# Kernel optimization log

Measured on AMD Instinct MI355X. Metric: run time of the kernel, lower is better.

The kernel has to match this reference:

```python
import jax, jax.numpy as jnp
import numpy as np
import math

NUM_CLASSES = 80
ANCHORS = [(12.0, 16.0), (19.0, 36.0), (40.0, 28.0)]
ANGLES = [-np.pi/3, -np.pi/6, 0.0, np.pi/6, np.pi/3, np.pi/2]
STRIDE = 8.0
SCALE_XY = 1.05
IGNORE_THRESH = 0.5
MASKED_ANCHORS = np.array([[w/STRIDE, h/STRIDE, a] for (w, h) in ANCHORS for a in ANGLES], dtype=np.float32)  # [18,3]
NA = MASKED_ANCHORS.shape[0]
LAMBDA_COORD, LAMBDA_CONF, LAMBDA_CLS = 1.0, 10.0, 1.0
FOCAL_ALPHA, FOCAL_GAMMA = 0.25, 2.0


def setup_inputs() -> dict:
    key = jax.random.key(0)
    B, G, nT = 8, 76, 240
    k1, k2, k3, k4, k5, k6 = jax.random.split(key, 6)
    output = jax.random.normal(k1, (B, NA * (NUM_CLASSES + 6), G, G), jnp.float32) * 0.1
    tb = jax.random.randint(k2, (nT,), 0, B).astype(jnp.float32)
    tl = jax.random.randint(k3, (nT,), 0, NUM_CLASSES).astype(jnp.float32)
    txy = jax.random.uniform(k4, (nT, 2), minval=0.02, maxval=0.98)
    twh = jax.random.uniform(k5, (nT, 2), minval=0.05, maxval=0.4)
    tang = jax.random.uniform(k6, (nT, 1), minval=-np.pi/2, maxval=np.pi/2)
    target = jnp.concatenate([tb[:, None], tl[:, None], txy, twh, tang], axis=-1)  # [nT,7]
    return {"output": output, "target": target}


def _smooth_l1(x, y):
    d = jnp.abs(x - y)
    return jnp.where(d < 1.0, 0.5 * d * d, d - 0.5)


def _bce(p, t):
    eps = 1e-7
    p = jnp.clip(p, eps, 1.0 - eps)
    return -(t * jnp.log(p) + (1.0 - t) * jnp.log(1.0 - p))


def _focal(p, t):
    loss = _bce(p, t)
    p_t = t * p + (1.0 - t) * (1.0 - p)
    alpha_f = t * FOCAL_ALPHA + (1.0 - t) * (1.0 - FOCAL_ALPHA)
    return loss * alpha_f * (1.0 - p_t) ** FOCAL_GAMMA


def _ciou(pb, tb):
    # pb, tb: [N,5] (cx, cy, w, h, angle) in grid units
    p1, p2 = pb[:, :2] - pb[:, 2:4] / 2, pb[:, :2] + pb[:, 2:4] / 2
    t1, t2 = tb[:, :2] - tb[:, 2:4] / 2, tb[:, :2] + tb[:, 2:4] / 2
    w1, h1 = p2[:, 0] - p1[:, 0], p2[:, 1] - p1[:, 1]
    w2, h2 = t2[:, 0] - t1[:, 0], t2[:, 1] - t1[:, 1]
    area1, area2 = w1 * h1, w2 * h2
    c1, c2 = (p1 + p2) / 2, (t1 + t2) / 2
    inter = jnp.clip(jnp.minimum(p2, t2) - jnp.maximum(p1, t1), 0.0)
    inter_area = inter[:, 0] * inter[:, 1]
    inter_diag = jnp.sum((c2 - c1) ** 2, axis=-1)
    outer = jnp.clip(jnp.maximum(p2, t2) - jnp.minimum(p1, t1), 0.0)
    outer_diag = outer[:, 0] ** 2 + outer[:, 1] ** 2
    union = area1 + area2 - inter_area
    u = inter_diag / outer_diag
    iou = inter_area / union
    v = (4.0 / math.pi ** 2) * (jnp.arctan(w2 / h2) - jnp.arctan(w1 / h1)) ** 2
    alpha = jax.lax.stop_gradient(v / ((1.0 - iou) + v))
    ciou = jnp.clip(iou - (u + alpha * v), -1.0, 1.0)
    skew_iou = iou * jnp.abs(jnp.cos(pb[:, 4] - tb[:, 4]))
    return skew_iou, ciou


def _forward(output, target):
    B, G = output.shape[0], output.shape[2]
    nC = NUM_CLASSES
    ma = jnp.asarray(MASKED_ANCHORS)
    pred = output.reshape(B, NA, nC + 6, G, G).transpose(0, 1, 3, 4, 2)  # [B,A,G,G,C+6]
    px = jax.nn.sigmoid(pred[..., 0]) * SCALE_XY - (SCALE_XY - 1) / 2
    py = jax.nn.sigmoid(pred[..., 1]) * SCALE_XY - (SCALE_XY - 1) / 2
    pw, ph, pa = pred[..., 2], pred[..., 3], pred[..., 4]
    pconf = jax.nn.sigmoid(pred[..., 5])
    pcls = jax.nn.sigmoid(pred[..., 6:])
    gx = jnp.arange(G, dtype=output.dtype)[None, None, None, :]
    gy = jnp.arange(G, dtype=output.dtype)[None, None, :, None]
    aw = ma[:, 0].reshape(1, NA, 1, 1)
    ah = ma[:, 1].reshape(1, NA, 1, 1)
    aa = ma[:, 2].reshape(1, NA, 1, 1)
    pred_boxes = jnp.stack([px + gx, py + gy, jnp.exp(pw) * aw, jnp.exp(ph) * ah, pa + aa], axis=-1)  # [B,A,G,G,5]
    out_dec = jnp.concatenate([
        jnp.concatenate([pred_boxes[..., :4] * STRIDE, pred_boxes[..., 4:]], axis=-1).reshape(B, -1, 5),
        pconf.reshape(B, -1, 1),
        pcls.reshape(B, -1, nC)], axis=-1)

    # ---- build_targets ----
    tgt_boxes = jnp.concatenate([target[:, 2:6] * G, target[:, 6:]], axis=-1)  # [nT,5]
    gxy, gwh, ga = tgt_boxes[:, :2], tgt_boxes[:, 2:4], tgt_boxes[:, 4]
    aw_, ah_, aa_ = ma[:, 0][:, None], ma[:, 1][:, None], ma[:, 2][:, None]  # [A,1]
    w2, h2 = gwh[:, 0][None, :], gwh[:, 1][None, :]                          # [1,nT]
    inter = jnp.minimum(aw_, w2) * jnp.minimum(ah_, h2)
    union = aw_ * ah_ + 1e-16 + w2 * h2 - inter
    offset = jnp.abs(aa_ - ga[None, :])                                       # [A,nT]
    arious = (inter / union) * jnp.abs(jnp.cos(aa_ - ga[None, :]))            # [A,nT]
    best_n = jnp.argmax(arious, axis=0)                                       # [nT]
    b = target[:, 0].astype(jnp.int32)
    labels = target[:, 1].astype(jnp.int32)
    gi = gxy[:, 0].astype(jnp.int32)
    gj = gxy[:, 1].astype(jnp.int32)

    zeros = jnp.zeros((B, NA, G, G), output.dtype)
    obj = zeros.at[b, best_n, gj, gi].set(1.0)
    noobj = jnp.ones((B, NA, G, G), output.dtype)
    cond = (arious > IGNORE_THRESH) | ((arious > 0.4) & (offset < np.pi / 12))  # [A,nT]
    a_idx = jnp.broadcast_to(jnp.arange(NA)[:, None], arious.shape)
    bb = jnp.broadcast_to(b[None, :], arious.shape)
    gjb = jnp.broadcast_to(gj[None, :], arious.shape)
    gib = jnp.broadcast_to(gi[None, :], arious.shape)
    noobj = noobj.at[bb, a_idx, gjb, gib].min(jnp.where(cond, 0.0, 1.0))
    noobj = noobj.at[b, best_n, gj, gi].set(0.0)

    ta_grid = zeros.at[b, best_n, gj, gi].set(ga - ma[best_n, 2])
    tcls = jnp.zeros((B, NA, G, G, nC), output.dtype).at[b, best_n, gj, gi, labels].set(1.0)
    tconf = obj

    pb = pred_boxes[b, best_n, gj, gi]  # [nT,5]
    iou, ciou = _ciou(pb, tgt_boxes)
    img_size = STRIDE * G
    bbox_scale = jax.lax.stop_gradient(2.0 - gwh[:, 0] * gwh[:, 1] / img_size ** 2)
    ciou_t = bbox_scale * (1.0 - ciou)

    class_ok = (jnp.argmax(pcls[b, best_n, gj, gi], axis=-1) == labels).astype(output.dtype)
    class_mask = zeros.at[b, best_n, gj, gi].set(class_ok)
    iou_scores = zeros.at[b, best_n, gj, gi].set(iou)
    skew = zeros.at[b, best_n, gj, gi].set(jnp.exp(1.0 - iou) - 1.0)
    ciou_grid = zeros.at[b, best_n, gj, gi].set(ciou_t)

    # ---- losses (masked means replace boolean indexing) ----
    n_obj = jnp.maximum(jnp.sum(obj), 1.0)
    n_noobj = jnp.maximum(jnp.sum(noobj), 1.0)
    reg = _smooth_l1(pa, ta_grid) + ciou_grid
    reg_const = jax.lax.stop_gradient(skew / jnp.where(obj > 0, reg, 1.0))
    reg_loss = jnp.sum(reg * reg_const * obj) / n_obj
    fl = _focal(pconf, tconf)
    conf_loss = jnp.sum(fl * obj) / n_obj + jnp.sum(fl * noobj) / n_noobj
    cls_loss = jnp.sum(_bce(pcls, tcls) * obj[..., None]) / (n_obj * nC)
    total_loss = LAMBDA_COORD * reg_loss + LAMBDA_CONF * conf_loss + LAMBDA_CLS * cls_loss
    return out_dec, total_loss


def reference(output, target):
    return _forward(output, target)
```

## Files before the change

### kernel.cpp

```cpp
#include <hip/hip_runtime.h>
#include <math.h>

#define NCLS 80
#define NANC 18
#define NB 8
#define GG 76
#define SS (GG*GG)
#define CHN (NCLS+6)
#define NCELL (NB*NANC*SS)
#define FLAG_WORDS ((NCELL+31)/32)
#define NT_MAX 240
#define TILE 64
#define NTILES ((SS+TILE-1)/TILE)
#define LSTR 65
#define PI_ 3.14159265358979323846

#define WS_WIN   64
#define WS_META  1024
#define WS_LM    4864
#define WS_FLAGS 6784
#define ZERO_WORDS ((WS_FLAGS + FLAG_WORDS*4)/4)

__device__ __constant__ float d_ma[NANC][3] = {
  {1.5f, 2.0f, (float)(-PI_/3)}, {1.5f, 2.0f, (float)(-PI_/6)}, {1.5f, 2.0f, 0.0f},
  {1.5f, 2.0f, (float)(PI_/6)},  {1.5f, 2.0f, (float)(PI_/3)},  {1.5f, 2.0f, (float)(PI_/2)},
  {2.375f, 4.5f, (float)(-PI_/3)}, {2.375f, 4.5f, (float)(-PI_/6)}, {2.375f, 4.5f, 0.0f},
  {2.375f, 4.5f, (float)(PI_/6)},  {2.375f, 4.5f, (float)(PI_/3)},  {2.375f, 4.5f, (float)(PI_/2)},
  {5.0f, 3.5f, (float)(-PI_/3)}, {5.0f, 3.5f, (float)(-PI_/6)}, {5.0f, 3.5f, 0.0f},
  {5.0f, 3.5f, (float)(PI_/6)},  {5.0f, 3.5f, (float)(PI_/3)},  {5.0f, 3.5f, (float)(PI_/2)},
};

__device__ __forceinline__ float sigm(float x) { return 1.0f / (1.0f + expf(-x)); }
__device__ __forceinline__ float fsig(float x) {
  return __builtin_amdgcn_rcpf(1.0f + __expf(-x));
}

__global__ void k_zero(unsigned* __restrict__ w, int n) {
  int i = blockIdx.x * blockDim.x + threadIdx.x;
  if (i < n) w[i] = 0u;
}

__global__ __launch_bounds__(256) void k_prep(const float* __restrict__ tgt,
                                              unsigned* __restrict__ flags,
                                              int* __restrict__ win,
                                              int4* __restrict__ meta,
                                              uint2* __restrict__ lmout,
                                              int* __restrict__ cnt, int nT) {
  __shared__ int s_key[NT_MAX], s_lab[NT_MAX];
  __shared__ int s_win[NT_MAX];
  __shared__ int s_zero;

  int t = threadIdx.x;
  if (t == 0) s_zero = 0;
  int bi = 0, gi = 0, gj = 0, bn = 0;
  unsigned cm = 0;
  if (t < nT) {
    float bf = tgt[t*7+0], lf = tgt[t*7+1];
    float gx = tgt[t*7+2] * (float)GG, gy = tgt[t*7+3] * (float)GG;
    float gw = tgt[t*7+4] * (float)GG, gh = tgt[t*7+5] * (float)GG;
    float ga = tgt[t*7+6];
    bi = (int)bf; gi = (int)gx; gj = (int)gy;
    int lab = (int)lf;
    float best = -1e30f;
    for (int a = 0; a < NANC; ++a) {
      float aw = d_ma[a][0], ah = d_ma[a][1], aa = d_ma[a][2];
      float inter = fminf(aw, gw) * fminf(ah, gh);
      float uni = aw*ah + 1e-16f + gw*gh - inter;
      float off = fabsf(aa - ga);
      float ar = inter / uni * fabsf(cosf(aa - ga));
      if (ar > best) { best = ar; bn = a; }
      if (ar > 0.5f || (ar > 0.4f && off < (float)(PI_/12))) cm |= (1u << a);
    }
    s_key[t] = ((bi*NANC + bn)*GG + gj)*GG + gi;
    s_lab[t] = lab;
    s_win[t] = 0;
  }
  __syncthreads();

  if (t < nT) {
    for (int a = 0; a < NANC; ++a) {
      if (((cm >> a) & 1u) || a == bn) {
        int cell = ((bi*NANC + a)*GG + gj)*GG + gi;
        unsigned bit = 1u << (cell & 31);
        unsigned old = atomicOr(&flags[cell >> 5], bit);
        if (!(old & bit)) atomicAdd(&s_zero, 1);
      }
    }
    int key = s_key[t];
    bool winner = true;
    for (int t2 = t + 1; t2 < nT; ++t2) if (s_key[t2] == key) { winner = false; break; }
    if (winner) {
      s_win[t] = 1;
      unsigned long long lm0 = 0, lm1 = 0;
      for (int t2 = 0; t2 < nT; ++t2) if (s_key[t2] == key) {
        int L = s_lab[t2];
        if (L < 64) lm0 |= 1ull << L; else lm1 |= 1ull << (L - 64);
      }
      lmout[t] = make_uint2((unsigned)(lm0 & 0xffffffffull), (unsigned)(lm0 >> 32));
      meta[t] = make_int4(bi, bn, gi, gj | ((int)(lm1 & 0xffffu) << 16));
      win[t] = 1;
    } else {
      win[t] = 0;
    }
  }
  __syncthreads();
  if (t == 0) {
    int nw = 0;
    for (int i = 0; i < nT; ++i) nw += s_win[i];
    cnt[0] = s_zero; cnt[1] = nw;
  }
}

__global__ __launch_bounds__(128) void k_cls(const float* __restrict__ tgt,
                                             const float* __restrict__ in,
                                             const int* __restrict__ win,
                                             const int4* __restrict__ meta,
                                             const uint2* __restrict__ lm,
                                             double* __restrict__ acc, int nT) {
  int t = blockIdx.x;
  if (t >= nT || !win[t]) return;
  int4 m = meta[t];
  int bi = m.x, bn = m.y, gi = m.z, gj = m.w & 0xffff;
  unsigned lmhi = ((unsigned)m.w) >> 16;
  uint2 l0 = lm[t];
  const float* base = in + ((size_t)(bi*NANC + bn)*CHN)*SS + (size_t)gj*GG + gi;
  int tid = threadIdx.x;

  float csum = 0.0f;
  if (tid < NCLS) {
    float p = fsig(base[(size_t)(6 + tid)*SS]);
    float pl = fminf(fmaxf(p, 1e-7f), 1.0f - 1e-7f);
    bool tc;
    if (tid < 32)      tc = (l0.x >> tid) & 1u;
    else if (tid < 64) tc = (l0.y >> (tid - 32)) & 1u;
    else               tc = (lmhi >> (tid - 64)) & 1u;
    csum = tc ? -__logf(pl) : -__logf(1.0f - pl);
  }
  for (int off = 32; off; off >>= 1) csum += __shfl_down(csum, off);
  if ((tid & 63) == 0) atomicAdd(&acc[3], (double)csum);

  if (tid == 96) {
    float gx = tgt[t*7+2] * (float)GG, gyv = tgt[t*7+3] * (float)GG;
    float gw = tgt[t*7+4] * (float)GG, gh = tgt[t*7+5] * (float)GG;
    float ga = tgt[t*7+6];
    float rx = base[0], ry = base[(size_t)SS], rw = base[2*(size_t)SS],
          rh = base[3*(size_t)SS], ra = base[4*(size_t)SS], rcf = base[5*(size_t)SS];
    float aw = d_ma[bn][0], ah = d_ma[bn][1], aa = d_ma[bn][2];
    float px = sigm(rx)*1.05f - 0.025f + (float)gi;
    float py = sigm(ry)*1.05f - 0.025f + (float)gj;
    float pw = expf(rw)*aw, ph = expf(rh)*ah;
    float pang = ra + aa;
    float p1x = px - pw*0.5f, p1y = py - ph*0.5f, p2x = px + pw*0.5f, p2y = py + ph*0.5f;
    float t1x = gx - gw*0.5f, t1y = gyv - gh*0.5f, t2x = gx + gw*0.5f, t2y = gyv + gh*0.5f;
    float w1 = p2x - p1x, h1 = p2y - p1y, w2 = t2x - t1x, h2 = t2y - t1y;
    float area1 = w1*h1, area2 = w2*h2;
    float c1x = (p1x+p2x)*0.5f, c1y = (p1y+p2y)*0.5f, c2x = (t1x+t2x)*0.5f, c2y = (t1y+t2y)*0.5f;
    float ix = fmaxf(fminf(p2x,t2x) - fmaxf(p1x,t1x), 0.0f);
    float iy = fmaxf(fminf(p2y,t2y) - fmaxf(p1y,t1y), 0.0f);
    float inter_area = ix*iy;
    float dcx = c2x - c1x, dcy = c2y - c1y;
    float inter_diag = dcx*dcx + dcy*dcy;
    float ox = fmaxf(fmaxf(p2x,t2x) - fminf(p1x,t1x), 0.0f);
    float oy = fmaxf(fmaxf(p2y,t2y) - fminf(p1y,t1y), 0.0f);
    float outer_diag = ox*ox + oy*oy;
    float uni = area1 + area2 - inter_area;
    float u = inter_diag / outer_diag;
    float iou = inter_area / uni;
    float da = atanf(w2/h2) - atanf(w1/h1);
    float v = (float)(4.0/(PI_*PI_)) * da * da;
    float alpha = v / (1.0f - iou + v);
    float ciou = fminf(fmaxf(iou - (u + alpha*v), -1.0f), 1.0f);
    float skew_iou = iou * fabsf(cosf(pang - ga));
    float skew = expf(1.0f - skew_iou) - 1.0f;
    float bscale = 2.0f - gw*gh/369664.0f;
    float ciou_t = bscale * (1.0f - ciou);
    float ta = ga - aa;
    float d = fabsf(ra - ta);
    float sl1 = (d < 1.0f) ? 0.5f*d*d : d - 0.5f;
    float reg = sl1 + ciou_t;
    atomicAdd(&acc[2], (double)(reg * (skew / reg)));
    float pc = sigm(rcf);
    float pcl = fminf(fmaxf(pc, 1e-7f), 1.0f - 1e-7f);
    float om = 1.0f - pc;
    atomicAdd(&acc[1], (double)(-logf(pcl) * 0.25f * om * om));
  }
}

__global__ __launch_bounds__(256) void k_main(const float* __restrict__ in,
                                              float* __restrict__ out,
                                              const unsigned* __restrict__ flags,
                                              double* __restrict__ acc) {
  __shared__ float lds[CHN * LSTR];
  int blk = blockIdx.x;
  int tile = blk % NTILES;
  int ba = blk / NTILES;
  int a = ba % NANC, b = ba / NANC;
  int s0 = tile * TILE;
  int count = min(TILE, SS - s0);
  int cnt4 = count >> 2;
  int sh = (count == TILE) ? 4 : 2;
  int tot4 = CHN * cnt4;

  const float* inb = in + ((size_t)(b*NANC + a)*CHN)*SS + s0;

  float4 r[6];
  #pragma unroll
  for (int k = 0; k < 6; ++k) {
    int i = threadIdx.x + k*256;
    if (i < tot4) {
      int c = i >> sh, s4 = i & (cnt4 - 1);
      r[k] = *(const float4*)(inb + (size_t)c*SS + 4*s4);
    }
  }
  #pragma unroll
  for (int k = 0; k < 6; ++k) {
    int i = threadIdx.x + k*256;
    if (i < tot4) {
      int c = i >> sh, s4 = i & (cnt4 - 1);
      float* p = &lds[c*LSTR + 4*s4];
      p[0] = r[k].x; p[1] = r[k].y; p[2] = r[k].z; p[3] = r[k].w;
    }
  }
  __syncthreads();

  if (threadIdx.x < 64) {
    int s = threadIdx.x;
    double fl = 0.0;
    if (s < count) {
      int spos = s0 + s;
      int gy = spos / GG, gx = spos - gy*GG;
      float aw = d_ma[a][0], ah = d_ma[a][1], aa = d_ma[a][2];
      lds[0*LSTR+s] = (fsig(lds[0*LSTR+s])*1.05f - 0.025f + (float)gx) * 8.0f;
      lds[1*LSTR+s] = (fsig(lds[1*LSTR+s])*1.05f - 0.025f + (float)gy) * 8.0f;
      lds[2*LSTR+s] = __expf(lds[2*LSTR+s]) * aw * 8.0f;
      lds[3*LSTR+s] = __expf(lds[3*LSTR+s]) * ah * 8.0f;
      lds[4*LSTR+s] = lds[4*LSTR+s] + aa;
      float p = fsig(lds[5*LSTR+s]);
      int cell = (b*NANC + a)*SS + spos;
      if (!((flags[cell >> 5] >> (cell & 31)) & 1u)) {
        float pcl = fminf(fmaxf(p, 1e-7f), 1.0f - 1e-7f);
        fl = (double)(-__logf(1.0f - pcl) * 0.75f * p * p);
      }
    }
    for (int off = 32; off; off >>= 1) fl += __shfl_down(fl, off);
    if (threadIdx.x == 0 && fl != 0.0) atomicAdd(&acc[0], fl);
  }
  __syncthreads();

  int np = count * (CHN/2);
  float2* outb2 = (float2*)(out + ((size_t)(b*NANC + a)*SS + s0)*CHN);
  for (int o2 = threadIdx.x; o2 < np; o2 += 256) {
    int s = o2 / (CHN/2);
    int h = o2 - s*(CHN/2);
    float v0 = lds[(2*h    )*LSTR + s];
    float v1 = lds[(2*h + 1)*LSTR + s];
    float r0 = (h < 3) ? v0 : fsig(v0);
    float r1 = (h < 2) ? v1 : fsig(v1);
    outb2[o2] = make_float2(r0, r1);
  }
}

__global__ void k_fin(const double* __restrict__ acc, const int* __restrict__ cnt,
                      float* __restrict__ out) {
  double n_obj = fmax((double)cnt[1], 1.0);
  double n_noobj = fmax((double)(NCELL - cnt[0]), 1.0);
  double reg_loss = acc[2] / n_obj;
  double conf_loss = acc[1] / n_obj + acc[0] / n_noobj;
  double cls_loss = acc[3] / (n_obj * (double)NCLS);
  out[(size_t)NCELL * CHN] = (float)(reg_loss + 10.0*conf_loss + cls_loss);
}

extern "C" void kernel_launch(void* const* d_in, const int* in_sizes, int n_in,
                              void* d_out, int out_size, void* d_ws, size_t ws_size,
                              hipStream_t stream) {
  const float* in  = (const float*)d_in[0];
  const float* tgt = (const float*)d_in[1];
  float* out = (float*)d_out;
  double* acc = (double*)d_ws;
  int* cnt = (int*)((char*)d_ws + 32);
  int* win = (int*)((char*)d_ws + WS_WIN);
  int4* meta = (int4*)((char*)d_ws + WS_META);
  uint2* lm = (uint2*)((char*)d_ws + WS_LM);
  unsigned* flags = (unsigned*)((char*)d_ws + WS_FLAGS);
  int nT = in_sizes[1] / 7;
  if (nT > NT_MAX) nT = NT_MAX;

  hipLaunchKernelGGL(k_zero, dim3((ZERO_WORDS + 255)/256), dim3(256), 0, stream,
                     (unsigned*)d_ws, ZERO_WORDS);
  hipLaunchKernelGGL(k_prep, dim3(1), dim3(256), 0, stream, tgt, flags, win, meta, lm, cnt, nT);
  hipLaunchKernelGGL(k_cls, dim3(nT), dim3(128), 0, stream, tgt, in, win, meta, lm, acc, nT);
  hipLaunchKernelGGL(k_main, dim3(NB*NANC*NTILES), dim3(256), 0, stream, in, out, flags, acc);
  hipLaunchKernelGGL(k_fin, dim3(1), dim3(1), 0, stream, acc, cnt, out);
}
```

Before: 250.5 us.

## Split noobj conf loss into loss kernel; row-aligned tiles with register prefetch in main

```diff
diff --git a/kernel.cpp b/kernel.cpp
--- a/kernel.cpp
+++ b/kernel.cpp
@@ -10,9 +10,14 @@
 #define NCELL (NB*NANC*SS)
 #define FLAG_WORDS ((NCELL+31)/32)
 #define NT_MAX 240
-#define TILE 64
-#define NTILES ((SS+TILE-1)/TILE)
-#define LSTR 65
+#define TILE 76
+#define LSTR 77
+#define TPB 4
+#define TGRP (GG/TPB)
+#define NLOAD 7
+#define TOT4 (CHN*(TILE/4))
+#define NCONF4 (NCELL/4)
+#define NCONFBLK ((NCONF4+255)/256)
 #define PI_ 3.14159265358979323846
 
 #define WS_WIN   64
@@ -111,152 +116,183 @@
   }
 }
 
-__global__ __launch_bounds__(128) void k_cls(const float* __restrict__ tgt,
-                                             const float* __restrict__ in,
-                                             const int* __restrict__ win,
-                                             const int4* __restrict__ meta,
-                                             const uint2* __restrict__ lm,
-                                             double* __restrict__ acc, int nT) {
-  int t = blockIdx.x;
-  if (t >= nT || !win[t]) return;
-  int4 m = meta[t];
-  int bi = m.x, bn = m.y, gi = m.z, gj = m.w & 0xffff;
-  unsigned lmhi = ((unsigned)m.w) >> 16;
-  uint2 l0 = lm[t];
-  const float* base = in + ((size_t)(bi*NANC + bn)*CHN)*SS + (size_t)gj*GG + gi;
+__global__ __launch_bounds__(256) void k_loss(const float* __restrict__ tgt,
+                                              const float* __restrict__ in,
+                                              const int* __restrict__ win,
+                                              const int4* __restrict__ meta,
+                                              const uint2* __restrict__ lm,
+                                              const unsigned* __restrict__ flags,
+                                              double* __restrict__ acc, int nT) {
+  int blk = blockIdx.x;
   int tid = threadIdx.x;
 
-  float csum = 0.0f;
-  if (tid < NCLS) {
-    float p = fsig(base[(size_t)(6 + tid)*SS]);
-    float pl = fminf(fmaxf(p, 1e-7f), 1.0f - 1e-7f);
-    bool tc;
-    if (tid < 32)      tc = (l0.x >> tid) & 1u;
-    else if (tid < 64) tc = (l0.y >> (tid - 32)) & 1u;
-    else               tc = (lmhi >> (tid - 64)) & 1u;
-    csum = tc ? -__logf(pl) : -__logf(1.0f - pl);
-  }
-  for (int off = 32; off; off >>= 1) csum += __shfl_down(csum, off);
-  if ((tid & 63) == 0) atomicAdd(&acc[3], (double)csum);
-
-  if (tid == 96) {
-    float gx = tgt[t*7+2] * (float)GG, gyv = tgt[t*7+3] * (float)GG;
-    float gw = tgt[t*7+4] * (float)GG, gh = tgt[t*7+5] * (float)GG;
-    float ga = tgt[t*7+6];
-    float rx = base[0], ry = base[(size_t)SS], rw = base[2*(size_t)SS],
-          rh = base[3*(size_t)SS], ra = base[4*(size_t)SS], rcf = base[5*(size_t)SS];
-    float aw = d_ma[bn][0], ah = d_ma[bn][1], aa = d_ma[bn][2];
-    float px = sigm(rx)*1.05f - 0.025f + (float)gi;
-    float py = sigm(ry)*1.05f - 0.025f + (float)gj;
-    float pw = expf(rw)*aw, ph = expf(rh)*ah;
-    float pang = ra + aa;
-    float p1x = px - pw*0.5f, p1y = py - ph*0.5f, p2x = px + pw*0.5f, p2y = py + ph*0.5f;
-    float t1x = gx - gw*0.5f, t1y = gyv - gh*0.5f, t2x = gx + gw*0.5f, t2y = gyv + gh*0.5f;
-    float w1 = p2x - p1x, h1 = p2y - p1y, w2 = t2x - t1x, h2 = t2y - t1y;
-    float area1 = w1*h1, area2 = w2*h2;
-    float c1x = (p1x+p2x)*0.5f, c1y = (p1y+p2y)*0.5f, c2x = (t1x+t2x)*0.5f, c2y = (t1y+t2y)*0.5f;
-    float ix = fmaxf(fminf(p2x,t2x) - fmaxf(p1x,t1x), 0.0f);
-    float iy = fmaxf(fminf(p2y,t2y) - fmaxf(p1y,t1y), 0.0f);
-    float inter_area = ix*iy;
-    float dcx = c2x - c1x, dcy = c2y - c1y;
-    float inter_diag = dcx*dcx + dcy*dcy;
-    float ox = fmaxf(fmaxf(p2x,t2x) - fminf(p1x,t1x), 0.0f);
-    float oy = fmaxf(fmaxf(p2y,t2y) - fminf(p1y,t1y), 0.0f);
-    float outer_diag = ox*ox + oy*oy;
-    float uni = area1 + area2 - inter_area;
-    float u = inter_diag / outer_diag;
-    float iou = inter_area / uni;
-    float da = atanf(w2/h2) - atanf(w1/h1);
-    float v = (float)(4.0/(PI_*PI_)) * da * da;
-    float alpha = v / (1.0f - iou + v);
-    float ciou = fminf(fmaxf(iou - (u + alpha*v), -1.0f), 1.0f);
-    float skew_iou = iou * fabsf(cosf(pang - ga));
-    float skew = expf(1.0f - skew_iou) - 1.0f;
-    float bscale = 2.0f - gw*gh/369664.0f;
-    float ciou_t = bscale * (1.0f - ciou);
-    float ta = ga - aa;
-    float d = fabsf(ra - ta);
-    float sl1 = (d < 1.0f) ? 0.5f*d*d : d - 0.5f;
-    float reg = sl1 + ciou_t;
-    atomicAdd(&acc[2], (double)(reg * (skew / reg)));
-    float pc = sigm(rcf);
-    float pcl = fminf(fmaxf(pc, 1e-7f), 1.0f - 1e-7f);
-    float om = 1.0f - pc;
-    atomicAdd(&acc[1], (double)(-logf(pcl) * 0.25f * om * om));
+  if (blk < nT) {
+    int t = blk;
+    if (!win[t]) return;
+    int4 m = meta[t];
+    int bi = m.x, bn = m.y, gi = m.z, gj = m.w & 0xffff;
+    unsigned lmhi = ((unsigned)m.w) >> 16;
+    uint2 l0 = lm[t];
+    const float* base = in + ((size_t)(bi*NANC + bn)*CHN)*SS + (size_t)gj*GG + gi;
+
+    float csum = 0.0f;
+    if (tid < NCLS) {
+      float p = fsig(base[(size_t)(6 + tid)*SS]);
+      float pl = fminf(fmaxf(p, 1e-7f), 1.0f - 1e-7f);
+      bool tc;
+      if (tid < 32)      tc = (l0.x >> tid) & 1u;
+      else if (tid < 64) tc = (l0.y >> (tid - 32)) & 1u;
+      else               tc = (lmhi >> (tid - 64)) & 1u;
+      csum = tc ? -__logf(pl) : -__logf(1.0f - pl);
+    }
+    for (int off = 32; off; off >>= 1) csum += __shfl_down(csum, off);
+    if ((tid & 63) == 0 && tid < 128) atomicAdd(&acc[3], (double)csum);
+
+    if (tid == 128) {
+      float gx = tgt[t*7+2] * (float)GG, gyv = tgt[t*7+3] * (float)GG;
+      float gw = tgt[t*7+4] * (float)GG, gh = tgt[t*7+5] * (float)GG;
+      float ga = tgt[t*7+6];
+      float rx = base[0], ry = base[(size_t)SS], rw = base[2*(size_t)SS],
+            rh = base[3*(size_t)SS], ra = base[4*(size_t)SS], rcf = base[5*(size_t)SS];
+      float aw = d_ma[bn][0], ah = d_ma[bn][1], aa = d_ma[bn][2];
+      float px = sigm(rx)*1.05f - 0.025f + (float)gi;
+      float py = sigm(ry)*1.05f - 0.025f + (float)gj;
+      float pw = expf(rw)*aw, ph = expf(rh)*ah;
+      float pang = ra + aa;
+      float p1x = px - pw*0.5f, p1y = py - ph*0.5f, p2x = px + pw*0.5f, p2y = py + ph*0.5f;
+      float t1x = gx - gw*0.5f, t1y = gyv - gh*0.5f, t2x = gx + gw*0.5f, t2y = gyv + gh*0.5f;
+      float w1 = p2x - p1x, h1 = p2y - p1y, w2 = t2x - t1x, h2 = t2y - t1y;
+      float area1 = w1*h1, area2 = w2*h2;
+      float c1x = (p1x+p2x)*0.5f, c1y = (p1y+p2y)*0.5f, c2x = (t1x+t2x)*0.5f, c2y = (t1y+t2y)*0.5f;
+      float ix = fmaxf(fminf(p2x,t2x) - fmaxf(p1x,t1x), 0.0f);
+      float iy = fmaxf(fminf(p2y,t2y) - fmaxf(p1y,t1y), 0.0f);
+      float inter_area = ix*iy;
+      float dcx = c2x - c1x, dcy = c2y - c1y;
+      float inter_diag = dcx*dcx + dcy*dcy;
+      float ox = fmaxf(fmaxf(p2x,t2x) - fminf(p1x,t1x), 0.0f);
+      float oy = fmaxf(fmaxf(p2y,t2y) - fminf(p1y,t1y), 0.0f);
+      float outer_diag = ox*ox + oy*oy;
+      float uni = area1 + area2 - inter_area;
+      float u = inter_diag / outer_diag;
+      float iou = inter_area / uni;
+      float da = atanf(w2/h2) - atanf(w1/h1);
+      float v = (float)(4.0/(PI_*PI_)) * da * da;
+      float alpha = v / (1.0f - iou + v);
+      float ciou = fminf(fmaxf(iou - (u + alpha*v), -1.0f), 1.0f);
+      float skew_iou = iou * fabsf(cosf(pang - ga));
+      float skew = expf(1.0f - skew_iou) - 1.0f;
+      float bscale = 2.0f - gw*gh/369664.0f;
+      float ciou_t = bscale * (1.0f - ciou);
+      float ta = ga - aa;
+      float d = fabsf(ra - ta);
+      float sl1 = (d < 1.0f) ? 0.5f*d*d : d - 0.5f;
+      float reg = sl1 + ciou_t;
+      atomicAdd(&acc[2], (double)(reg * (skew / reg)));
+      float pc = sigm(rcf);
+      float pcl = fminf(fmaxf(pc, 1e-7f), 1.0f - 1e-7f);
+      float om = 1.0f - pc;
+      atomicAdd(&acc[1], (double)(-logf(pcl) * 0.25f * om * om));
+    }
+    return;
+  }
+
+  __shared__ double wsum[4];
+  int j = (blk - nT)*256 + tid;
+  double fl = 0.0;
+  if (j < NCONF4) {
+    int ba = j / (SS/4);
+    int q  = j - ba*(SS/4);
+    int spos = 4*q;
+    const float4 v4 = *(const float4*)(in + (size_t)ba*CHN*SS + 5*(size_t)SS + spos);
+    int cell0 = ba*SS + spos;
+    unsigned word = flags[cell0 >> 5];
+    int bbit = cell0 & 31;
+    float pv[4] = {v4.x, v4.y, v4.z, v4.w};
+    #pragma unroll
+    for (int e = 0; e < 4; ++e) {
+      if (!((word >> (bbit + e)) & 1u)) {
+        float p = fsig(pv[e]);
+        float pcl = fminf(fmaxf(p, 1e-7f), 1.0f - 1e-7f);
+        fl += (double)(-__logf(1.0f - pcl) * 0.75f * p * p);
+      }
+    }
+  }
+  int lane = tid & 63, wid = tid >> 6;
+  for (int off = 32; off; off >>= 1) fl += __shfl_down(fl, off);
+  if (lane == 0) wsum[wid] = fl;
+  __syncthreads();
+  if (tid == 0) {
+    double s = wsum[0] + wsum[1] + wsum[2] + wsum[3];
+    if (s != 0.0) atomicAdd(&acc[0], s);
   }
 }
 
 __global__ __launch_bounds__(256) void k_main(const float* __restrict__ in,
-                                              float* __restrict__ out,
-                                              const unsigned* __restrict__ flags,
-                                              double* __restrict__ acc) {
+                                              float* __restrict__ out) {
   __shared__ float lds[CHN * LSTR];
   int blk = blockIdx.x;
-  int tile = blk % NTILES;
-  int ba = blk / NTILES;
-  int a = ba % NANC, b = ba / NANC;
-  int s0 = tile * TILE;
-  int count = min(TILE, SS - s0);
-  int cnt4 = count >> 2;
-  int sh = (count == TILE) ? 4 : 2;
-  int tot4 = CHN * cnt4;
-
-  const float* inb = in + ((size_t)(b*NANC + a)*CHN)*SS + s0;
-
-  float4 r[6];
-  #pragma unroll
-  for (int k = 0; k < 6; ++k) {
-    int i = threadIdx.x + k*256;
-    if (i < tot4) {
-      int c = i >> sh, s4 = i & (cnt4 - 1);
-      r[k] = *(const float4*)(inb + (size_t)c*SS + 4*s4);
-    }
-  }
-  #pragma unroll
-  for (int k = 0; k < 6; ++k) {
-    int i = threadIdx.x + k*256;
-    if (i < tot4) {
-      int c = i >> sh, s4 = i & (cnt4 - 1);
-      float* p = &lds[c*LSTR + 4*s4];
-      p[0] = r[k].x; p[1] = r[k].y; p[2] = r[k].z; p[3] = r[k].w;
-    }
-  }
-  __syncthreads();
-
-  if (threadIdx.x < 64) {
-    int s = threadIdx.x;
-    double fl = 0.0;
-    if (s < count) {
-      int spos = s0 + s;
-      int gy = spos / GG, gx = spos - gy*GG;
-      float aw = d_ma[a][0], ah = d_ma[a][1], aa = d_ma[a][2];
-      lds[0*LSTR+s] = (fsig(lds[0*LSTR+s])*1.05f - 0.025f + (float)gx) * 8.0f;
-      lds[1*LSTR+s] = (fsig(lds[1*LSTR+s])*1.05f - 0.025f + (float)gy) * 8.0f;
-      lds[2*LSTR+s] = __expf(lds[2*LSTR+s]) * aw * 8.0f;
-      lds[3*LSTR+s] = __expf(lds[3*LSTR+s]) * ah * 8.0f;
-      lds[4*LSTR+s] = lds[4*LSTR+s] + aa;
-      float p = fsig(lds[5*LSTR+s]);
-      int cell = (b*NANC + a)*SS + spos;
-      if (!((flags[cell >> 5] >> (cell & 31)) & 1u)) {
-        float pcl = fminf(fmaxf(p, 1e-7f), 1.0f - 1e-7f);
-        fl = (double)(-__logf(1.0f - pcl) * 0.75f * p * p);
-      }
-    }
-    for (int off = 32; off; off >>= 1) fl += __shfl_down(fl, off);
-    if (threadIdx.x == 0 && fl != 0.0) atomicAdd(&acc[0], fl);
-  }
-  __syncthreads();
-
-  int np = count * (CHN/2);
-  float2* outb2 = (float2*)(out + ((size_t)(b*NANC + a)*SS + s0)*CHN);
-  for (int o2 = threadIdx.x; o2 < np; o2 += 256) {
-    int s = o2 / (CHN/2);
-    int h = o2 - s*(CHN/2);
-    float v0 = lds[(2*h    )*LSTR + s];
-    float v1 = lds[(2*h + 1)*LSTR + s];
-    float r0 = (h < 3) ? v0 : fsig(v0);
-    float r1 = (h < 2) ? v1 : fsig(v1);
-    outb2[o2] = make_float2(r0, r1);
+  int tgrp = blk % TGRP;
+  int ba = blk / TGRP;
+  int a = ba % NANC;
+  float aw8 = d_ma[a][0] * 8.0f, ah8 = d_ma[a][1] * 8.0f, aa = d_ma[a][2];
+
+  const float* plane_in = in + (size_t)ba * CHN * SS;
+  float* plane_out = out + (size_t)ba * SS * CHN;
+
+  int tile0 = tgrp * TPB;
+  float4 r[NLOAD];
+
+  {
+    const float* tin = plane_in + tile0 * TILE;
+    #pragma unroll
+    for (int k = 0; k < NLOAD; ++k) {
+      int i = threadIdx.x + k*256;
+      if (i < TOT4) {
+        int c = i / (TILE/4), s4 = i - c*(TILE/4);
+        r[k] = *(const float4*)(tin + (size_t)c*SS + 4*s4);
+      }
+    }
+  }
+
+  for (int tt = 0; tt < TPB; ++tt) {
+    int tile = tile0 + tt;
+    __syncthreads();
+    #pragma unroll
+    for (int k = 0; k < NLOAD; ++k) {
+      int i = threadIdx.x + k*256;
+      if (i < TOT4) {
+        int c = i / (TILE/4), s4 = i - c*(TILE/4);
+        float* p = &lds[c*LSTR + 4*s4];
+        p[0] = r[k].x; p[1] = r[k].y; p[2] = r[k].z; p[3] = r[k].w;
+      }
+    }
+    __syncthreads();
+    if (tt + 1 < TPB) {
+      const float* tin = plane_in + (tile + 1) * TILE;
+      #pragma unroll
+      for (int k = 0; k < NLOAD; ++k) {
+        int i = threadIdx.x + k*256;
+        if (i < TOT4) {
+          int c = i / (TILE/4), s4 = i - c*(TILE/4);
+          r[k] = *(const float4*)(tin + (size_t)c*SS + 4*s4);
+        }
+      }
+    }
+    float gyf = (float)tile;
+    float2* outb2 = (float2*)(plane_out + (size_t)tile * TILE * CHN);
+    for (int o2 = threadIdx.x; o2 < TILE*(CHN/2); o2 += 256) {
+      int s = o2 / (CHN/2);
+      int h = o2 - s*(CHN/2);
+      float v0 = lds[(2*h    )*LSTR + s];
+      float v1 = lds[(2*h + 1)*LSTR + s];
+      float r0, r1;
+      if (h >= 3)      { r0 = fsig(v0); r1 = fsig(v1); }
+      else if (h == 0) { r0 = (fsig(v0)*1.05f - 0.025f + (float)s)*8.0f;
+                         r1 = (fsig(v1)*1.05f - 0.025f + gyf)*8.0f; }
+      else if (h == 1) { r0 = __expf(v0)*aw8; r1 = __expf(v1)*ah8; }
+      else             { r0 = v0 + aa; r1 = fsig(v1); }
+      outb2[o2] = make_float2(r0, r1);
+    }
   }
 }
 
@@ -288,7 +324,8 @@
   hipLaunchKernelGGL(k_zero, dim3((ZERO_WORDS + 255)/256), dim3(256), 0, stream,
                      (unsigned*)d_ws, ZERO_WORDS);
   hipLaunchKernelGGL(k_prep, dim3(1), dim3(256), 0, stream, tgt, flags, win, meta, lm, cnt, nT);
-  hipLaunchKernelGGL(k_cls, dim3(nT), dim3(128), 0, stream, tgt, in, win, meta, lm, acc, nT);
-  hipLaunchKernelGGL(k_main, dim3(NB*NANC*NTILES), dim3(256), 0, stream, in, out, flags, acc);
+  hipLaunchKernelGGL(k_loss, dim3(nT + NCONFBLK), dim3(256), 0, stream,
+                     tgt, in, win, meta, lm, flags, acc, nT);
   hipLaunchKernelGGL(k_fin, dim3(1), dim3(1), 0, stream, acc, cnt, out);
-}
+  hipLaunchKernelGGL(k_main, dim3(NB*NANC*TGRP), dim3(256), 0, stream, in, out);
+}
```

Result: faster. 208.8 us (-16.6%).
